# Performance work log

Hardware: AMD Instinct MI355X
Metric: run time of the kernel (lower is better)

Reference implementation:

```python
import jax, jax.numpy as jnp
import numpy as np

B, S, D, H = 2, 2048, 1024, 16
DK = D // H  # 64


def setup_inputs() -> dict:
    key = jax.random.key(0)
    ks = jax.random.split(key, 9)
    query = jax.random.normal(ks[0], (B, S, D), dtype=jnp.float32)
    k_in = jax.random.normal(ks[1], (B, S, D), dtype=jnp.float32)
    v_in = jax.random.normal(ks[2], (B, S, D), dtype=jnp.float32)
    mask = jax.random.randint(ks[3], (B, S, S), 0, 2, dtype=jnp.int32)
    sc = 1.0 / np.sqrt(D)
    Wq = jax.random.normal(ks[4], (H, D, DK), dtype=jnp.float32) * sc  # per-head q proj
    Wk = jax.random.normal(ks[5], (H, D, DK), dtype=jnp.float32) * sc
    Wv = jax.random.normal(ks[6], (H, D, DK), dtype=jnp.float32) * sc
    Wu = jax.random.normal(ks[7], (D, D), dtype=jnp.float32) * sc  # unifyheads weight
    bu = jax.random.normal(ks[8], (D,), dtype=jnp.float32) * 0.01
    return {"query": query, "key": k_in, "value": v_in, "mask": mask,
            "Wq": Wq, "Wk": Wk, "Wv": Wv, "Wu": Wu, "bu": bu}


def reference(query, key, value, mask, Wq, Wk, Wv, Wu, bu):
    scale = DK ** 0.25  # original divides q and k each by d_k^(1/4)
    q = jnp.einsum('bsd,hdk->bhsk', query, Wq) / scale
    k = jnp.einsum('bsd,hdk->bhsk', key, Wk) / scale
    v = jnp.einsum('bsd,hdk->bhsk', value, Wv)
    scores = jnp.einsum('bhsk,bhtk->bhst', q, k)  # [B,H,S,S]
    scores = jnp.where(mask[:, None, :, :] == 0, jnp.float32(-1e9), scores)
    attn = jax.nn.softmax(scores, axis=-1)
    out = jnp.einsum('bhst,bhtk->bhsk', attn, v)
    out = jnp.transpose(out, (0, 2, 1, 3)).reshape(query.shape[0], query.shape[1], D)  # concat heads
    return out @ Wu + bu
```

## Files before the change

kernel.cpp:

```cpp
#include <hip/hip_runtime.h>
#include <hip/hip_bf16.h>


typedef __bf16 bf16_t;
typedef __attribute__((ext_vector_type(4))) __bf16 bf16x4;
typedef __attribute__((ext_vector_type(8))) __bf16 bf16x8;
typedef __attribute__((ext_vector_type(4))) float f32x4;
typedef unsigned int u32;

#define B_ 2
#define S_ 2048
#define D_ 1024
#define H_ 16
#define DK_ 64
#define NX_ (4096 * 1024)

static __device__ __forceinline__ f32x4 mfma16(bf16x8 a, bf16x8 b, f32x4 c) {
  return __builtin_amdgcn_mfma_f32_16x16x32_bf16(a, b, c, 0, 0, 0);
}

static __device__ __forceinline__ void async16(const bf16_t* g, bf16_t* l) {
  __builtin_amdgcn_global_load_lds(
      (const __attribute__((address_space(1))) u32*)g,
      (__attribute__((address_space(3))) u32*)l, 16, 0, 0);
}

__global__ __launch_bounds__(256) void cvt_x(const float* __restrict__ q,
                                             const float* __restrict__ k,
                                             const float* __restrict__ v,
                                             bf16_t* __restrict__ qo,
                                             bf16_t* __restrict__ ko,
                                             bf16_t* __restrict__ vo) {
  const int z = blockIdx.y;
  const float* src = (z == 0) ? q : (z == 1) ? k : v;
  bf16_t* dst = (z == 0) ? qo : (z == 1) ? ko : vo;
  size_t i = ((size_t)blockIdx.x * 256 + threadIdx.x) * 8;
  float4 a = *(const float4*)(src + i);
  float4 b = *(const float4*)(src + i + 4);
  bf16x8 o;
  o[0] = (bf16_t)a.x; o[1] = (bf16_t)a.y; o[2] = (bf16_t)a.z; o[3] = (bf16_t)a.w;
  o[4] = (bf16_t)b.x; o[5] = (bf16_t)b.y; o[6] = (bf16_t)b.z; o[7] = (bf16_t)b.w;
  *(bf16x8*)(dst + i) = o;
}

__global__ __launch_bounds__(256) void wtrans(
    const float* __restrict__ Wq, const float* __restrict__ Wk,
    const float* __restrict__ Wv, const float* __restrict__ Wu,
    bf16_t* __restrict__ Bq, bf16_t* __restrict__ Bk,
    bf16_t* __restrict__ Bv, bf16_t* __restrict__ Bu, float qkscale) {
  __shared__ __align__(16) bf16_t T[64][72];
  const int z = blockIdx.z;
  const float* W = (z == 0) ? Wq : (z == 1) ? Wk : (z == 2) ? Wv : Wu;
  bf16_t* BT = (z == 0) ? Bq : (z == 1) ? Bk : (z == 2) ? Bv : Bu;
  const float scale = (z <= 1) ? qkscale : 1.0f;
  const int d0 = blockIdx.x * 64, nt = blockIdx.y;
  const int tid = threadIdx.x;
  const int r = tid & 63, g = tid >> 6;

  const float* src = (z < 3)
      ? W + ((size_t)nt * D_ + d0 + r) * DK_ + g * 16
      : W + (size_t)(d0 + r) * D_ + nt * 64 + g * 16;
#pragma unroll
  for (int j = 0; j < 4; ++j) {
    float4 w4 = *(const float4*)(src + j * 4);
    T[g * 16 + j * 4 + 0][r] = (bf16_t)(w4.x * scale);
    T[g * 16 + j * 4 + 1][r] = (bf16_t)(w4.y * scale);
    T[g * 16 + j * 4 + 2][r] = (bf16_t)(w4.z * scale);
    T[g * 16 + j * 4 + 3][r] = (bf16_t)(w4.w * scale);
  }
  __syncthreads();
  const int orow = tid >> 3, seg = tid & 7;
#pragma unroll
  for (int p = 0; p < 2; ++p) {
    int rr = p * 32 + orow;
    *(bf16x8*)(BT + (size_t)(nt * 64 + rr) * D_ + d0 + seg * 8) =
        *(const bf16x8*)&T[rr][seg * 8];
  }
}

__global__ __launch_bounds__(256) void vt_build(const bf16_t* __restrict__ V,
                                                bf16_t* __restrict__ Vt) {
  __shared__ __align__(16) bf16_t T[64][72];
  const int r0 = blockIdx.x * 64;
  const int c0 = blockIdx.y * 64;
  const int tid = threadIdx.x;
#pragma unroll
  for (int it = 0; it < 2; ++it) {
    int t = tid + it * 256;
    int rr = t >> 3, cc = (t & 7) * 8;
    *(bf16x8*)&T[rr][cc] = *(const bf16x8*)(V + (size_t)(r0 + rr) * D_ + c0 + cc);
  }
  __syncthreads();
#pragma unroll
  for (int it = 0; it < 2; ++it) {
    int t = tid + it * 256;
    int cr = t >> 3, rc = (t & 7) * 8;
    bf16x8 v;
#pragma unroll
    for (int j = 0; j < 8; ++j) v[j] = T[rc + j][cr];
    *(bf16x8*)(Vt + (size_t)(c0 + cr) * 4096 + r0 + rc) = v;
  }
}

__global__ __launch_bounds__(256) void mask_pack(const int* __restrict__ mask,
                                                 unsigned int* __restrict__ bits) {
  int w = blockIdx.x * 256 + threadIdx.x;
  const int4* p = (const int4*)(mask + (size_t)w * 32);
  unsigned int v = 0;
#pragma unroll
  for (int i = 0; i < 8; ++i) {
    int4 m4 = p[i];
    v |= (m4.x != 0 ? 1u : 0u) << (i * 4 + 0);
    v |= (m4.y != 0 ? 1u : 0u) << (i * 4 + 1);
    v |= (m4.z != 0 ? 1u : 0u) << (i * 4 + 2);
    v |= (m4.w != 0 ? 1u : 0u) << (i * 4 + 3);
  }
  bits[w] = v;
}

__global__ __launch_bounds__(256) void gemm_bt(
    const bf16_t* __restrict__ A0, const bf16_t* __restrict__ A1,
    const bf16_t* __restrict__ A2, const bf16_t* __restrict__ BT0,
    const bf16_t* __restrict__ BT1, const bf16_t* __restrict__ BT2,
    bf16_t* __restrict__ C0, bf16_t* __restrict__ C1, bf16_t* __restrict__ C2) {
  __shared__ __align__(16) bf16_t As[128 * 64];
  __shared__ __align__(16) bf16_t Bs[128 * 64];

  const int z = blockIdx.z;
  const bf16_t* A = (z == 0) ? A0 : (z == 1) ? A1 : A2;
  const bf16_t* BT = (z == 0) ? BT0 : (z == 1) ? BT1 : BT2;
  bf16_t* C = (z == 0) ? C0 : (z == 1) ? C1 : C2;

  const int tid = threadIdx.x;
  const int lane = tid & 63, wave = tid >> 6;
  const int l = lane & 15, quad = lane >> 4;
  const int wm = wave >> 1, wn = wave & 1;
  const int row0 = blockIdx.x * 128, col0 = blockIdx.y * 128;

  const int lr = lane >> 3;
  const int gc8 = (lane & 7) ^ lr;
  const int xl = l & 7;

  f32x4 acc[4][4];
#pragma unroll
  for (int i = 0; i < 4; ++i)
#pragma unroll
    for (int j = 0; j < 4; ++j) acc[i][j] = {0.f, 0.f, 0.f, 0.f};

  for (int k0 = 0; k0 < 1024; k0 += 64) {
    __syncthreads();
#pragma unroll
    for (int c = 0; c < 4; ++c) {
      int r = wave * 32 + c * 8;
      async16(A + (size_t)(row0 + r + lr) * 1024 + k0 + gc8 * 8, As + r * 64);
      async16(BT + (size_t)(col0 + r + lr) * 1024 + k0 + gc8 * 8, Bs + r * 64);
    }
    __syncthreads();

#pragma unroll
    for (int kh = 0; kh < 2; ++kh) {
      bf16x8 af[4], bf[4];
#pragma unroll
      for (int f = 0; f < 4; ++f)
        af[f] = *(const bf16x8*)&As[(wm * 64 + f * 16 + l) * 64 +
                                    (((kh * 4 + quad) ^ xl) * 8)];
#pragma unroll
      for (int f = 0; f < 4; ++f)
        bf[f] = *(const bf16x8*)&Bs[(wn * 64 + f * 16 + l) * 64 +
                                    (((kh * 4 + quad) ^ xl) * 8)];
#pragma unroll
      for (int fm = 0; fm < 4; ++fm)
#pragma unroll
        for (int fn = 0; fn < 4; ++fn)
          acc[fm][fn] = mfma16(af[fm], bf[fn], acc[fm][fn]);
    }
  }

#pragma unroll
  for (int fm = 0; fm < 4; ++fm)
#pragma unroll
    for (int fn = 0; fn < 4; ++fn)
#pragma unroll
      for (int reg = 0; reg < 4; ++reg) {
        int row = row0 + wm * 64 + fm * 16 + quad * 4 + reg;
        int col = col0 + wn * 64 + fn * 16 + l;
        C[(size_t)row * 1024 + col] = (bf16_t)acc[fm][fn][reg];
      }
}

__global__ __launch_bounds__(256) void gemm_bt64(
    const bf16_t* __restrict__ A, const bf16_t* __restrict__ BT,
    float* __restrict__ C, const float* __restrict__ bias) {
  __shared__ __align__(16) bf16_t As[64 * 64];
  __shared__ __align__(16) bf16_t Bs[128 * 64];

  const int tid = threadIdx.x;
  const int lane = tid & 63, wave = tid >> 6;
  const int l = lane & 15, quad = lane >> 4;
  const int row0 = blockIdx.x * 64, col0 = blockIdx.y * 128;

  const int lr = lane >> 3;
  const int gc8 = (lane & 7) ^ lr;
  const int xl = l & 7;

  f32x4 acc[4][2];
#pragma unroll
  for (int i = 0; i < 4; ++i)
#pragma unroll
    for (int j = 0; j < 2; ++j) acc[i][j] = {0.f, 0.f, 0.f, 0.f};

  for (int k0 = 0; k0 < 1024; k0 += 64) {
    __syncthreads();
#pragma unroll
    for (int c = 0; c < 2; ++c) {
      int r = wave * 16 + c * 8;
      async16(A + (size_t)(row0 + r + lr) * 1024 + k0 + gc8 * 8, As + r * 64);
    }
#pragma unroll
    for (int c = 0; c < 4; ++c) {
      int r = wave * 32 + c * 8;
      async16(BT + (size_t)(col0 + r + lr) * 1024 + k0 + gc8 * 8, Bs + r * 64);
    }
    __syncthreads();

#pragma unroll
    for (int kh = 0; kh < 2; ++kh) {
      bf16x8 af[4], bf[2];
#pragma unroll
      for (int f = 0; f < 4; ++f)
        af[f] = *(const bf16x8*)&As[(f * 16 + l) * 64 +
                                    (((kh * 4 + quad) ^ xl) * 8)];
#pragma unroll
      for (int f = 0; f < 2; ++f)
        bf[f] = *(const bf16x8*)&Bs[(wave * 32 + f * 16 + l) * 64 +
                                    (((kh * 4 + quad) ^ xl) * 8)];
#pragma unroll
      for (int fm = 0; fm < 4; ++fm)
#pragma unroll
        for (int fn = 0; fn < 2; ++fn)
          acc[fm][fn] = mfma16(af[fm], bf[fn], acc[fm][fn]);
    }
  }

#pragma unroll
  for (int fm = 0; fm < 4; ++fm)
#pragma unroll
    for (int fn = 0; fn < 2; ++fn)
#pragma unroll
      for (int reg = 0; reg < 4; ++reg) {
        int row = row0 + fm * 16 + quad * 4 + reg;
        int col = col0 + wave * 32 + fn * 16 + l;
        C[(size_t)row * 1024 + col] = acc[fm][fn][reg] + bias[col];
      }
}

__global__ __launch_bounds__(256, 2) void attn_kernel(
    const bf16_t* __restrict__ Qx, const bf16_t* __restrict__ Kx,
    const bf16_t* __restrict__ Vt, const unsigned int* __restrict__ mbits,
    bf16_t* __restrict__ out) {
  __shared__ __align__(16) bf16_t Ks[2][64 * 64];
  __shared__ __align__(16) bf16_t Vts[2][64 * 64];
  __shared__ __align__(16) bf16_t Ps[4][32][72];

  const int tid = threadIdx.x;
  const int lane = tid & 63, wave = tid >> 6;
  const int l = lane & 15, quad = lane >> 4;

  const int flat = blockIdx.x + 16 * (blockIdx.y + 16 * blockIdx.z);
  const int serial = (flat >> 3) + (flat & 7) * 64;
  const int qt = serial & 15;
  const int h = (serial >> 4) & 15;
  const int b = serial >> 8;

  const int ch = h * 64;
  const size_t rb = (size_t)b * S_;
  const int q0 = qt * 128 + wave * 32;
  const int quad4 = quad * 4;

  const int lr = lane >> 3;
  const int gc8 = (lane & 7) ^ lr;
  const int xl = l & 7;

  bf16x8 bq[2][2];
#pragma unroll
  for (int mf = 0; mf < 2; ++mf) {
    const bf16_t* qp = Qx + (rb + q0 + mf * 16 + l) * D_ + ch;
    bq[mf][0] = *(const bf16x8*)(qp + quad * 8);
    bq[mf][1] = *(const bf16x8*)(qp + 32 + quad * 8);
  }

  bf16x8 ones;
#pragma unroll
  for (int j = 0; j < 8; ++j) ones[j] = (bf16_t)1.0f;

  const f32x4 zero = {0.f, 0.f, 0.f, 0.f};
  f32x4 o[2][4];
  f32x4 rs[2];
#pragma unroll
  for (int mf = 0; mf < 2; ++mf) {
    rs[mf] = zero;
#pragma unroll
    for (int nt = 0; nt < 4; ++nt) o[mf][nt] = zero;
  }

  const u32* mrow[2];
#pragma unroll
  for (int mf = 0; mf < 2; ++mf)
    mrow[mf] = mbits + (size_t)(b * S_ + q0 + mf * 16 + l) * (S_ / 32);

  auto stage = [&](int t0, int buf) {
#pragma unroll
    for (int it = 0; it < 2; ++it) {
      int r0 = it * 32 + wave * 8;
      async16(Kx + (rb + t0 + r0 + lr) * D_ + ch + gc8 * 8,
              &Ks[buf][r0 * 64]);
      async16(Vt + (size_t)(ch + r0 + lr) * 4096 + rb + t0 + gc8 * 8,
              &Vts[buf][r0 * 64]);
    }
  };

  stage(0, 0);
  uint2 mwc[2] = {*(const uint2*)&mrow[0][0], *(const uint2*)&mrow[1][0]};

  int cur = 0;
  for (int t0 = 0; t0 < S_; t0 += 64) {
    __syncthreads();
    const int tn = t0 + 64;
    if (tn < S_) stage(tn, cur ^ 1);
    const int nidx = (tn < S_) ? (tn >> 5) : 0;
    uint2 mwn0 = *(const uint2*)&mrow[0][nidx];
    uint2 mwn1 = *(const uint2*)&mrow[1][nidx];

    const bf16_t* Kc = Ks[cur];
    const bf16_t* Vc = Vts[cur];

#pragma unroll
    for (int ts = 0; ts < 4; ++ts) {
      int rK = (ts * 16 + l) * 64;
      bf16x8 ak0 = *(const bf16x8*)&Kc[rK + ((quad ^ xl) * 8)];
      bf16x8 ak1 = *(const bf16x8*)&Kc[rK + (((4 + quad) ^ xl) * 8)];
      int base = (ts & 1) * 16 + quad4;
#pragma unroll
      for (int mf = 0; mf < 2; ++mf) {
        f32x4 s = mfma16(ak0, bq[mf][0], zero);
        s = mfma16(ak1, bq[mf][1], s);
        u32 mw = (ts < 2) ? mwc[mf].x : mwc[mf].y;
        bf16x4 pv;
#pragma unroll
        for (int reg = 0; reg < 4; ++reg) {
          float e = exp2f(s[reg]);
          int bm = __builtin_amdgcn_sbfe(mw, base + reg, 1);
          float p = __int_as_float(__float_as_int(e) & bm);
          pv[reg] = (bf16_t)p;
        }
        *(bf16x4*)&Ps[wave][mf * 16 + l][ts * 16 + quad4] = pv;
      }
    }

    bf16x8 ap[2][2];
#pragma unroll
    for (int mf = 0; mf < 2; ++mf) {
      ap[mf][0] = *(const bf16x8*)&Ps[wave][mf * 16 + l][quad * 8];
      ap[mf][1] = *(const bf16x8*)&Ps[wave][mf * 16 + l][32 + quad * 8];
    }

    __builtin_amdgcn_s_setprio(1);
#pragma unroll
    for (int mf = 0; mf < 2; ++mf) {
      rs[mf] = mfma16(ap[mf][0], ones, rs[mf]);
      rs[mf] = mfma16(ap[mf][1], ones, rs[mf]);
    }
#pragma unroll
    for (int nt = 0; nt < 4; ++nt) {
      int rV = (nt * 16 + l) * 64;
      bf16x8 bv0 = *(const bf16x8*)&Vc[rV + ((quad ^ xl) * 8)];
      bf16x8 bv1 = *(const bf16x8*)&Vc[rV + (((4 + quad) ^ xl) * 8)];
#pragma unroll
      for (int mf = 0; mf < 2; ++mf) {
        o[mf][nt] = mfma16(ap[mf][0], bv0, o[mf][nt]);
        o[mf][nt] = mfma16(ap[mf][1], bv1, o[mf][nt]);
      }
    }
    __builtin_amdgcn_s_setprio(0);

    mwc[0] = mwn0;
    mwc[1] = mwn1;
    cur ^= 1;
  }

#pragma unroll
  for (int mf = 0; mf < 2; ++mf) {
#pragma unroll
    for (int reg = 0; reg < 4; ++reg) {
      float inv = (rs[mf][reg] > 0.f) ? (1.f / rs[mf][reg]) : 0.f;
      int srow = q0 + mf * 16 + quad4 + reg;
      bf16_t* op = out + (rb + srow) * D_ + ch;
#pragma unroll
      for (int nt = 0; nt < 4; ++nt)
        op[nt * 16 + l] = (bf16_t)(o[mf][nt][reg] * inv);
    }
  }
}

extern "C" void kernel_launch(void* const* d_in, const int* in_sizes, int n_in,
                              void* d_out, int out_size, void* d_ws, size_t ws_size,
                              hipStream_t stream) {
  const float* q_in = (const float*)d_in[0];
  const float* k_in = (const float*)d_in[1];
  const float* v_in = (const float*)d_in[2];
  const int* mask = (const int*)d_in[3];
  const float* Wq = (const float*)d_in[4];
  const float* Wk = (const float*)d_in[5];
  const float* Wv = (const float*)d_in[6];
  const float* Wu = (const float*)d_in[7];
  const float* bu = (const float*)d_in[8];
  float* outp = (float*)d_out;

  bf16_t* qx = (bf16_t*)d_ws;
  bf16_t* kx = qx + NX_;
  bf16_t* vx = kx + NX_;
  bf16_t* qb = vx + NX_;
  bf16_t* kb = qb + NX_;
  bf16_t* vb = kb + NX_;
  bf16_t* BTq = vb + NX_;
  bf16_t* BTk = BTq + D_ * D_;
  bf16_t* BTv = BTk + D_ * D_;
  bf16_t* BTu = BTv + D_ * D_;
  unsigned int* mb = (unsigned int*)(BTu + D_ * D_);
  bf16_t* ab = qx;
  bf16_t* vtb = kx;

  const float qkscale = 0.35355339059327373f * 1.2011224087864498f;

  dim3 blk(256);
  cvt_x<<<dim3(2048, 3), blk, 0, stream>>>(q_in, k_in, v_in, qx, kx, vx);
  wtrans<<<dim3(16, 16, 4), blk, 0, stream>>>(Wq, Wk, Wv, Wu, BTq, BTk, BTv, BTu, qkscale);
  mask_pack<<<dim3(1024), blk, 0, stream>>>(mask, mb);
  gemm_bt<<<dim3(32, 8, 3), blk, 0, stream>>>(qx, kx, vx, BTq, BTk, BTv,
                                              qb, kb, vb);
  vt_build<<<dim3(64, 16), blk, 0, stream>>>(vb, vtb);
  attn_kernel<<<dim3(S_ / 128, H_, B_), dim3(256), 0, stream>>>(qb, kb, vtb, mb, ab);
  gemm_bt64<<<dim3(64, 8), blk, 0, stream>>>(ab, BTu, outp, bu);
}
```

Measured before the change: 273.9 us.

## Merge prep kernels and compute V projection transposed to drop vt_build

The three preprocessing kernels (activation cast, weight transpose, mask packing) are merged into one launch using a flat block index. The V projection is computed with operands swapped (weights times activations) so the GEMM writes V already transposed with a 4096 leading dimension, which removes the separate vt_build transpose kernel and its extra memory pass. This cuts two launches and one global read and write of V. It adds branching in the combined prep kernel, and the transposed-output stores may be less coalesced.

```diff
diff --git a/kernel.cpp b/kernel.cpp
--- a/kernel.cpp
+++ b/kernel.cpp
@@ -25,97 +25,71 @@
       (__attribute__((address_space(3))) u32*)l, 16, 0, 0);
 }
 
-__global__ __launch_bounds__(256) void cvt_x(const float* __restrict__ q,
-                                             const float* __restrict__ k,
-                                             const float* __restrict__ v,
-                                             bf16_t* __restrict__ qo,
-                                             bf16_t* __restrict__ ko,
-                                             bf16_t* __restrict__ vo) {
-  const int z = blockIdx.y;
-  const float* src = (z == 0) ? q : (z == 1) ? k : v;
-  bf16_t* dst = (z == 0) ? qo : (z == 1) ? ko : vo;
-  size_t i = ((size_t)blockIdx.x * 256 + threadIdx.x) * 8;
-  float4 a = *(const float4*)(src + i);
-  float4 b = *(const float4*)(src + i + 4);
-  bf16x8 o;
-  o[0] = (bf16_t)a.x; o[1] = (bf16_t)a.y; o[2] = (bf16_t)a.z; o[3] = (bf16_t)a.w;
-  o[4] = (bf16_t)b.x; o[5] = (bf16_t)b.y; o[6] = (bf16_t)b.z; o[7] = (bf16_t)b.w;
-  *(bf16x8*)(dst + i) = o;
-}
-
-__global__ __launch_bounds__(256) void wtrans(
+__global__ __launch_bounds__(256) void prep(
+    const float* __restrict__ q, const float* __restrict__ k,
+    const float* __restrict__ v, const int* __restrict__ mask,
     const float* __restrict__ Wq, const float* __restrict__ Wk,
     const float* __restrict__ Wv, const float* __restrict__ Wu,
-    bf16_t* __restrict__ Bq, bf16_t* __restrict__ Bk,
-    bf16_t* __restrict__ Bv, bf16_t* __restrict__ Bu, float qkscale) {
+    bf16_t* __restrict__ qo, bf16_t* __restrict__ ko, bf16_t* __restrict__ vo,
+    bf16_t* __restrict__ Bq, bf16_t* __restrict__ Bk, bf16_t* __restrict__ Bv,
+    bf16_t* __restrict__ Bu, unsigned int* __restrict__ bits, float qkscale) {
   __shared__ __align__(16) bf16_t T[64][72];
-  const int z = blockIdx.z;
-  const float* W = (z == 0) ? Wq : (z == 1) ? Wk : (z == 2) ? Wv : Wu;
-  bf16_t* BT = (z == 0) ? Bq : (z == 1) ? Bk : (z == 2) ? Bv : Bu;
-  const float scale = (z <= 1) ? qkscale : 1.0f;
-  const int d0 = blockIdx.x * 64, nt = blockIdx.y;
+  const int f = blockIdx.x;
   const int tid = threadIdx.x;
-  const int r = tid & 63, g = tid >> 6;
-
-  const float* src = (z < 3)
-      ? W + ((size_t)nt * D_ + d0 + r) * DK_ + g * 16
-      : W + (size_t)(d0 + r) * D_ + nt * 64 + g * 16;
-#pragma unroll
-  for (int j = 0; j < 4; ++j) {
-    float4 w4 = *(const float4*)(src + j * 4);
-    T[g * 16 + j * 4 + 0][r] = (bf16_t)(w4.x * scale);
-    T[g * 16 + j * 4 + 1][r] = (bf16_t)(w4.y * scale);
-    T[g * 16 + j * 4 + 2][r] = (bf16_t)(w4.z * scale);
-    T[g * 16 + j * 4 + 3][r] = (bf16_t)(w4.w * scale);
-  }
-  __syncthreads();
-  const int orow = tid >> 3, seg = tid & 7;
-#pragma unroll
-  for (int p = 0; p < 2; ++p) {
-    int rr = p * 32 + orow;
-    *(bf16x8*)(BT + (size_t)(nt * 64 + rr) * D_ + d0 + seg * 8) =
-        *(const bf16x8*)&T[rr][seg * 8];
-  }
-}
-
-__global__ __launch_bounds__(256) void vt_build(const bf16_t* __restrict__ V,
-                                                bf16_t* __restrict__ Vt) {
-  __shared__ __align__(16) bf16_t T[64][72];
-  const int r0 = blockIdx.x * 64;
-  const int c0 = blockIdx.y * 64;
-  const int tid = threadIdx.x;
-#pragma unroll
-  for (int it = 0; it < 2; ++it) {
-    int t = tid + it * 256;
-    int rr = t >> 3, cc = (t & 7) * 8;
-    *(bf16x8*)&T[rr][cc] = *(const bf16x8*)(V + (size_t)(r0 + rr) * D_ + c0 + cc);
-  }
-  __syncthreads();
-#pragma unroll
-  for (int it = 0; it < 2; ++it) {
-    int t = tid + it * 256;
-    int cr = t >> 3, rc = (t & 7) * 8;
-    bf16x8 v;
-#pragma unroll
-    for (int j = 0; j < 8; ++j) v[j] = T[rc + j][cr];
-    *(bf16x8*)(Vt + (size_t)(c0 + cr) * 4096 + r0 + rc) = v;
-  }
-}
-
-__global__ __launch_bounds__(256) void mask_pack(const int* __restrict__ mask,
-                                                 unsigned int* __restrict__ bits) {
-  int w = blockIdx.x * 256 + threadIdx.x;
-  const int4* p = (const int4*)(mask + (size_t)w * 32);
-  unsigned int v = 0;
-#pragma unroll
-  for (int i = 0; i < 8; ++i) {
-    int4 m4 = p[i];
-    v |= (m4.x != 0 ? 1u : 0u) << (i * 4 + 0);
-    v |= (m4.y != 0 ? 1u : 0u) << (i * 4 + 1);
-    v |= (m4.z != 0 ? 1u : 0u) << (i * 4 + 2);
-    v |= (m4.w != 0 ? 1u : 0u) << (i * 4 + 3);
-  }
-  bits[w] = v;
+
+  if (f < 6144) {
+    const int z = f / 2048, bx = f - z * 2048;
+    const float* src = (z == 0) ? q : (z == 1) ? k : v;
+    bf16_t* dst = (z == 0) ? qo : (z == 1) ? ko : vo;
+    size_t i = ((size_t)bx * 256 + tid) * 8;
+    float4 a = *(const float4*)(src + i);
+    float4 b = *(const float4*)(src + i + 4);
+    bf16x8 o;
+    o[0] = (bf16_t)a.x; o[1] = (bf16_t)a.y; o[2] = (bf16_t)a.z; o[3] = (bf16_t)a.w;
+    o[4] = (bf16_t)b.x; o[5] = (bf16_t)b.y; o[6] = (bf16_t)b.z; o[7] = (bf16_t)b.w;
+    *(bf16x8*)(dst + i) = o;
+  } else if (f < 7168) {
+    const int idx = f - 6144;
+    const int bx = idx & 15, by = (idx >> 4) & 15, z = idx >> 8;
+    const float* W = (z == 0) ? Wq : (z == 1) ? Wk : (z == 2) ? Wv : Wu;
+    bf16_t* BT = (z == 0) ? Bq : (z == 1) ? Bk : (z == 2) ? Bv : Bu;
+    const float scale = (z <= 1) ? qkscale : 1.0f;
+    const int d0 = bx * 64, nt = by;
+    const int r = tid & 63, g = tid >> 6;
+
+    const float* src = (z < 3)
+        ? W + ((size_t)nt * D_ + d0 + r) * DK_ + g * 16
+        : W + (size_t)(d0 + r) * D_ + nt * 64 + g * 16;
+#pragma unroll
+    for (int j = 0; j < 4; ++j) {
+      float4 w4 = *(const float4*)(src + j * 4);
+      T[g * 16 + j * 4 + 0][r] = (bf16_t)(w4.x * scale);
+      T[g * 16 + j * 4 + 1][r] = (bf16_t)(w4.y * scale);
+      T[g * 16 + j * 4 + 2][r] = (bf16_t)(w4.z * scale);
+      T[g * 16 + j * 4 + 3][r] = (bf16_t)(w4.w * scale);
+    }
+    __syncthreads();
+    const int orow = tid >> 3, seg = tid & 7;
+#pragma unroll
+    for (int p = 0; p < 2; ++p) {
+      int rr = p * 32 + orow;
+      *(bf16x8*)(BT + (size_t)(nt * 64 + rr) * D_ + d0 + seg * 8) =
+          *(const bf16x8*)&T[rr][seg * 8];
+    }
+  } else {
+    const int w = (f - 7168) * 256 + tid;
+    const int4* p = (const int4*)(mask + (size_t)w * 32);
+    unsigned int vv = 0;
+#pragma unroll
+    for (int i = 0; i < 8; ++i) {
+      int4 m4 = p[i];
+      vv |= (m4.x != 0 ? 1u : 0u) << (i * 4 + 0);
+      vv |= (m4.y != 0 ? 1u : 0u) << (i * 4 + 1);
+      vv |= (m4.z != 0 ? 1u : 0u) << (i * 4 + 2);
+      vv |= (m4.w != 0 ? 1u : 0u) << (i * 4 + 3);
+    }
+    bits[w] = vv;
+  }
 }
 
 __global__ __launch_bounds__(256) void gemm_bt(
@@ -127,15 +101,19 @@
   __shared__ __align__(16) bf16_t Bs[128 * 64];
 
   const int z = blockIdx.z;
+  const int gx = blockIdx.x;
   const bf16_t* A = (z == 0) ? A0 : (z == 1) ? A1 : A2;
   const bf16_t* BT = (z == 0) ? BT0 : (z == 1) ? BT1 : BT2;
   bf16_t* C = (z == 0) ? C0 : (z == 1) ? C1 : C2;
+  const int row_blk = (z < 2) ? (gx >> 3) : (gx & 7);
+  const int col_blk = (z < 2) ? (gx & 7) : (gx >> 3);
+  const size_t ldc = (z < 2) ? 1024 : 4096;
 
   const int tid = threadIdx.x;
   const int lane = tid & 63, wave = tid >> 6;
   const int l = lane & 15, quad = lane >> 4;
   const int wm = wave >> 1, wn = wave & 1;
-  const int row0 = blockIdx.x * 128, col0 = blockIdx.y * 128;
+  const int row0 = row_blk * 128, col0 = col_blk * 128;
 
   const int lr = lane >> 3;
   const int gc8 = (lane & 7) ^ lr;
@@ -184,7 +162,7 @@
       for (int reg = 0; reg < 4; ++reg) {
         int row = row0 + wm * 64 + fm * 16 + quad * 4 + reg;
         int col = col0 + wn * 64 + fn * 16 + l;
-        C[(size_t)row * 1024 + col] = (bf16_t)acc[fm][fn][reg];
+        C[(size_t)row * ldc + col] = (bf16_t)acc[fm][fn][reg];
       }
 }
 
@@ -421,24 +399,23 @@
   bf16_t* vx = kx + NX_;
   bf16_t* qb = vx + NX_;
   bf16_t* kb = qb + NX_;
-  bf16_t* vb = kb + NX_;
-  bf16_t* BTq = vb + NX_;
+  bf16_t* vtb = kb + NX_;
+  bf16_t* BTq = vtb + NX_;
   bf16_t* BTk = BTq + D_ * D_;
   bf16_t* BTv = BTk + D_ * D_;
   bf16_t* BTu = BTv + D_ * D_;
   unsigned int* mb = (unsigned int*)(BTu + D_ * D_);
   bf16_t* ab = qx;
-  bf16_t* vtb = kx;
 
   const float qkscale = 0.35355339059327373f * 1.2011224087864498f;
 
   dim3 blk(256);
-  cvt_x<<<dim3(2048, 3), blk, 0, stream>>>(q_in, k_in, v_in, qx, kx, vx);
-  wtrans<<<dim3(16, 16, 4), blk, 0, stream>>>(Wq, Wk, Wv, Wu, BTq, BTk, BTv, BTu, qkscale);
-  mask_pack<<<dim3(1024), blk, 0, stream>>>(mask, mb);
-  gemm_bt<<<dim3(32, 8, 3), blk, 0, stream>>>(qx, kx, vx, BTq, BTk, BTv,
-                                              qb, kb, vb);
-  vt_build<<<dim3(64, 16), blk, 0, stream>>>(vb, vtb);
-  attn_kernel<<<dim3(S_ / 128, H_, B_), dim3(256), 0, stream>>>(qb, kb, vtb, mb, ab);
+  prep<<<dim3(8192), blk, 0, stream>>>(q_in, k_in, v_in, mask,
+                                       Wq, Wk, Wv, Wu,
+                                       qx, kx, vx,
+                                       BTq, BTk, BTv, BTu, mb, qkscale);
+  gemm_bt<<<dim3(256, 1, 3), blk, 0, stream>>>(qx, kx, BTv, BTq, BTk, vx,
+                                               qb, kb, vtb);
+  attn_kernel<<<dim3(S_ / 128, H_, B_), blk, 0, stream>>>(qb, kb, vtb, mb, ab);
   gemm_bt64<<<dim3(64, 8), blk, 0, stream>>>(ab, BTu, outp, bu);
 }
```

After: 266.5 us. 2.7% less time.
